# Performance work log

Hardware: AMD Instinct MI355X
Metric: run time of the kernel (lower is better)

The kernel has to match this reference:

```python
import jax, jax.numpy as jnp
import numpy as np

B, S, D, H = 2, 2048, 1024, 16
DK = D // H  # 64


def setup_inputs() -> dict:
    key = jax.random.key(0)
    ks = jax.random.split(key, 5)
    query_input = jax.random.normal(ks[0], (B, S, D), dtype=jnp.float32)
    # additive mask: 1.0 where attention is disallowed (causal upper triangle)
    mask = jnp.triu(jnp.ones((S, S), dtype=jnp.float32), k=1)[None, None, :, :]
    scale = 1.0 / np.sqrt(D)
    wq = jax.random.normal(ks[1], (D, D), dtype=jnp.float32) * scale
    wk = jax.random.normal(ks[2], (D, D), dtype=jnp.float32) * scale
    wv = jax.random.normal(ks[3], (D, D), dtype=jnp.float32) * scale
    wo = jax.random.normal(ks[4], (D, D), dtype=jnp.float32) * scale
    return {"query_input": query_input, "mask": mask, "wq": wq, "wk": wk, "wv": wv, "wo": wo}


def _split_heads(x):
    # [B, S, D] -> [B, H, S, DK]
    b, s, _ = x.shape
    return x.reshape(b, s, H, DK).transpose(0, 2, 1, 3)


def reference(query_input, mask, wq, wk, wv, wo):
    # self-attention: key_input = value_input = query_input
    q = _split_heads(query_input @ wq)  # [B, H, S, DK]
    k = _split_heads(query_input @ wk)
    v = _split_heads(query_input @ wv)
    scores = jnp.einsum('bhqd,bhkd->bhqk', q, k) / jnp.sqrt(jnp.float32(DK))
    scores = scores + mask * (-1e9)
    attn = jax.nn.softmax(scores, axis=-1)
    out = jnp.einsum('bhqk,bhkd->bhqd', attn, v)  # [B, H, S, DK]
    out = out.transpose(0, 2, 1, 3).reshape(query_input.shape[0], -1, D)
    return out @ wo
```

## Files before the change

kernel.cpp:

```cpp
#include <hip/hip_runtime.h>

typedef __attribute__((ext_vector_type(8))) short bf16x8;
typedef __attribute__((ext_vector_type(4))) float f32x4;
typedef __attribute__((ext_vector_type(4))) unsigned short u16x4;

#define S_LEN 2048
#define D_DIM 1024
#define NHEAD 16
#define DK 64
#define BH 32
#define MROWS 4096

__device__ __forceinline__ unsigned short f2bf(float f) {
    unsigned int u = __float_as_uint(f);
    u += 0x7fffu + ((u >> 16) & 1u);
    return (unsigned short)(u >> 16);
}

__device__ __forceinline__ void gload16(const void* g, void* l) {
    __builtin_amdgcn_global_load_lds(
        (const __attribute__((address_space(1))) void*)g,
        (__attribute__((address_space(3))) void*)l, 16, 0, 0);
}

__global__ __launch_bounds__(256) void cast_x_kernel(const float* __restrict__ X,
                                                     unsigned short* __restrict__ Xb) {
    int idx = blockIdx.x * 256 + threadIdx.x;
    float4 v = ((const float4*)X)[idx];
    u16x4 o;
    o.x = f2bf(v.x); o.y = f2bf(v.y); o.z = f2bf(v.z); o.w = f2bf(v.w);
    ((u16x4*)Xb)[idx] = o;
}

__global__ __launch_bounds__(256) void wtrans_kernel(const float* __restrict__ wq,
                                                     const float* __restrict__ wk,
                                                     const float* __restrict__ wv,
                                                     const float* __restrict__ wo,
                                                     unsigned short* __restrict__ Wt) {
    int z = blockIdx.z;
    const float* W = (z == 0) ? wq : (z == 1) ? wk : (z == 2) ? wv : wo;
    unsigned short* O = Wt + (size_t)z * D_DIM * D_DIM;
    __shared__ float t[32][33];
    int tx = threadIdx.x, ty = threadIdx.y;
    int bx = blockIdx.x * 32;
    int by = blockIdx.y * 32;
#pragma unroll
    for (int i = 0; i < 4; ++i)
        t[ty + i * 8][tx] = W[(size_t)(by + ty + i * 8) * D_DIM + bx + tx];
    __syncthreads();
#pragma unroll
    for (int i = 0; i < 4; ++i)
        O[(size_t)(bx + ty + i * 8) * D_DIM + by + tx] = f2bf(t[tx][ty + i * 8]);
}

__device__ __forceinline__ void gemm_mainloop(const unsigned short* __restrict__ A,
                                              const unsigned short* __restrict__ Bt,
                                              int K, int m0, int n0,
                                              unsigned short* As, unsigned short* Bs,
                                              f32x4 acc[4][4]) {
    const int tid = threadIdx.x;
    const int lane = tid & 63, wid = tid >> 6;
    const int wr = wid >> 1, wc = wid & 1;
    const int fr = lane & 15, fk = (lane >> 4) * 8;
    for (int k0 = 0; k0 < K; k0 += 32) {
        __syncthreads();
#pragma unroll
        for (int c = 0; c < 2; ++c) {
            int idx = c * 256 + tid;
            int row = idx >> 2;
            int col = (idx & 3) * 8;
            int base = (c * 256 + wid * 64) * 8;
            gload16(&A[(size_t)(m0 + row) * K + k0 + col], &As[base]);
            gload16(&Bt[(size_t)(n0 + row) * K + k0 + col], &Bs[base]);
        }
        __syncthreads();
        bf16x8 af[4], bfr[4];
#pragma unroll
        for (int i = 0; i < 4; ++i)
            af[i] = *(const bf16x8*)&As[(wr * 64 + i * 16 + fr) * 32 + fk];
#pragma unroll
        for (int j = 0; j < 4; ++j)
            bfr[j] = *(const bf16x8*)&Bs[(wc * 64 + j * 16 + fr) * 32 + fk];
#pragma unroll
        for (int i = 0; i < 4; ++i)
#pragma unroll
            for (int j = 0; j < 4; ++j)
                acc[i][j] = __builtin_amdgcn_mfma_f32_16x16x32_bf16(af[i], bfr[j], acc[i][j], 0, 0, 0);
    }
}

#define QSCALE 0.18033688011112042f
__global__ __launch_bounds__(256) void gemm_qkv_kernel(const unsigned short* __restrict__ Xb,
                                                       const unsigned short* __restrict__ Wt,
                                                       unsigned short* __restrict__ QKV) {
    __shared__ __align__(16) unsigned short As[128 * 32];
    __shared__ __align__(16) unsigned short Bs[128 * 32];
    const unsigned short* Bt = Wt + (size_t)blockIdx.z * D_DIM * D_DIM;
    unsigned short* Out = QKV + (size_t)blockIdx.z * MROWS * D_DIM;
    int m0 = blockIdx.y * 128, n0 = blockIdx.x * 128;
    f32x4 acc[4][4] = {};
    gemm_mainloop(Xb, Bt, D_DIM, m0, n0, As, Bs, acc);
    const float qs = (blockIdx.z == 0) ? QSCALE : 1.0f;
    const int lane = threadIdx.x & 63, wid = threadIdx.x >> 6;
    const int wr = wid >> 1, wc = wid & 1;
#pragma unroll
    for (int i = 0; i < 4; ++i)
#pragma unroll
        for (int j = 0; j < 4; ++j)
#pragma unroll
            for (int r = 0; r < 4; ++r) {
                int gm = m0 + wr * 64 + i * 16 + (lane >> 4) * 4 + r;
                int gn = n0 + wc * 64 + j * 16 + (lane & 15);
                int b = gm >> 11, s = gm & 2047, h = gn >> 6, dk = gn & 63;
                Out[((size_t)((b * NHEAD + h) * S_LEN + s)) * DK + dk] = f2bf(acc[i][j][r] * qs);
            }
}

__global__ __launch_bounds__(256) void vtrans_kernel(const unsigned short* __restrict__ V,
                                                     unsigned short* __restrict__ Vt) {
    __shared__ unsigned short tile[64][65];
    int bh = blockIdx.y;
    int s0 = blockIdx.x * 64;
    int t = threadIdx.x;
#pragma unroll
    for (int i = 0; i < 16; ++i) {
        int idx = i * 256 + t;
        int row = idx >> 6, col = idx & 63;
        tile[row][col] = V[((size_t)bh * S_LEN + s0 + row) * DK + col];
    }
    __syncthreads();
#pragma unroll
    for (int i = 0; i < 16; ++i) {
        int idx = i * 256 + t;
        int dr = idx >> 6, sc = idx & 63;
        Vt[((size_t)bh * DK + dr) * S_LEN + s0 + sc] = tile[sc][dr];
    }
}

__global__ __launch_bounds__(256) void attn_kernel(const unsigned short* __restrict__ QKV,
                                                   const unsigned short* __restrict__ Vt,
                                                   unsigned short* __restrict__ AO) {
    const int bh = blockIdx.y;
    const int tid = threadIdx.x, lane = tid & 63, wid = tid >> 6;
    const int fr = lane & 15, fkg = lane >> 4, fk = fkg * 8;
    const unsigned short* Q = QKV;
    const unsigned short* Kd = QKV + (size_t)MROWS * D_DIM;

    __shared__ __align__(16) unsigned short Ks[2][64][64];
    __shared__ __align__(16) unsigned short Vs[2][64][64];
    __shared__ __align__(16) unsigned short Ps[4][16][64];

    const int b = bh >> 4, h = bh & 15;
    const int rsw  = fr & 7;
    const int off0 = (fkg ^ rsw) * 8;
    const int off1 = ((4 + fkg) ^ rsw) * 8;

    for (int half = 0; half < 2; ++half) {
        const int qi = half ? (31 - (int)blockIdx.x) : (int)blockIdx.x;
        const int q0 = qi * 64;
        const int qr = q0 + wid * 16;

        bf16x8 qf0 = *(const bf16x8*)&Q[((size_t)bh * S_LEN + qr + fr) * DK + fk];
        bf16x8 qf1 = *(const bf16x8*)&Q[((size_t)bh * S_LEN + qr + fr) * DK + 32 + fk];

        f32x4 o[4] = {};
        float m = -1e30f, l = 0.f;
        const int ntiles = qi + 1;
        int buf = 0;

#pragma unroll
        for (int c = 0; c < 2; ++c) {
            int chunk = wid * 128 + c * 64 + lane;
            int row = chunk >> 3;
            int scol = ((chunk & 7) ^ (row & 7)) * 8;
            int base = (wid * 128 + c * 64) * 8;
            gload16(&Kd[((size_t)bh * S_LEN + row) * DK + scol], &Ks[0][0][0] + base);
            gload16(&Vt[((size_t)bh * DK + row) * S_LEN + scol], &Vs[0][0][0] + base);
        }
        __syncthreads();

        for (int t = 0; t < ntiles; ++t) {
            if (t + 1 < ntiles) {
                const int ktn = (t + 1) * 64;
#pragma unroll
                for (int c = 0; c < 2; ++c) {
                    int chunk = wid * 128 + c * 64 + lane;
                    int row = chunk >> 3;
                    int scol = ((chunk & 7) ^ (row & 7)) * 8;
                    int base = (wid * 128 + c * 64) * 8;
                    gload16(&Kd[((size_t)bh * S_LEN + ktn + row) * DK + scol], &Ks[buf ^ 1][0][0] + base);
                    gload16(&Vt[((size_t)bh * DK + row) * S_LEN + ktn + scol], &Vs[buf ^ 1][0][0] + base);
                }
            }

            f32x4 s4[4];
#pragma unroll
            for (int nj = 0; nj < 4; ++nj) {
                const unsigned short* krow = &Ks[buf][nj * 16 + fr][0];
                bf16x8 kf0 = *(const bf16x8*)&krow[off0];
                bf16x8 kf1 = *(const bf16x8*)&krow[off1];
                f32x4 z = {};
                z = __builtin_amdgcn_mfma_f32_16x16x32_bf16(kf0, qf0, z, 0, 0, 0);
                z = __builtin_amdgcn_mfma_f32_16x16x32_bf16(kf1, qf1, z, 0, 0, 0);
                s4[nj] = z;
            }

            if (t == ntiles - 1) {
                const int qoff = wid * 16 + fr;
#pragma unroll
                for (int nj = 0; nj < 4; ++nj)
#pragma unroll
                    for (int r = 0; r < 4; ++r)
                        s4[nj][r] = (nj * 16 + fkg * 4 + r > qoff) ? -1e30f : s4[nj][r];
            }

            float m0_ = fmaxf(fmaxf(s4[0][0], s4[0][1]), fmaxf(s4[0][2], s4[0][3]));
            float m1_ = fmaxf(fmaxf(s4[1][0], s4[1][1]), fmaxf(s4[1][2], s4[1][3]));
            float m2_ = fmaxf(fmaxf(s4[2][0], s4[2][1]), fmaxf(s4[2][2], s4[2][3]));
            float m3_ = fmaxf(fmaxf(s4[3][0], s4[3][1]), fmaxf(s4[3][2], s4[3][3]));
            float mt = fmaxf(fmaxf(m0_, m1_), fmaxf(m2_, m3_));
            mt = fmaxf(mt, __shfl_xor(mt, 16, 64));
            mt = fmaxf(mt, __shfl_xor(mt, 32, 64));
            float mn = fmaxf(m, mt);
            float corr = exp2f(m - mn);
            m = mn;
            float ps = 0.f;
            u16x4 pw[4];
#pragma unroll
            for (int nj = 0; nj < 4; ++nj) {
                float p0 = exp2f(s4[nj][0] - mn);
                float p1 = exp2f(s4[nj][1] - mn);
                float p2 = exp2f(s4[nj][2] - mn);
                float p3 = exp2f(s4[nj][3] - mn);
                ps += (p0 + p1) + (p2 + p3);
                pw[nj].x = f2bf(p0); pw[nj].y = f2bf(p1);
                pw[nj].z = f2bf(p2); pw[nj].w = f2bf(p3);
            }
            ps += __shfl_xor(ps, 16, 64);
            ps += __shfl_xor(ps, 32, 64);
            l = l * corr + ps;
#pragma unroll
            for (int j = 0; j < 4; ++j) o[j] *= corr;

#pragma unroll
            for (int nj = 0; nj < 4; ++nj) {
                int chunk = nj * 2 + (fkg >> 1);
                int el = (fkg & 1) * 4;
                *(u16x4*)&Ps[wid][fr][((chunk ^ rsw) << 3) + el] = pw[nj];
            }
            bf16x8 pf0 = *(const bf16x8*)&Ps[wid][fr][off0];
            bf16x8 pf1 = *(const bf16x8*)&Ps[wid][fr][off1];
#pragma unroll
            for (int j = 0; j < 4; ++j) {
                const unsigned short* vrow = &Vs[buf][j * 16 + fr][0];
                bf16x8 vf0 = *(const bf16x8*)&vrow[off0];
                bf16x8 vf1 = *(const bf16x8*)&vrow[off1];
                o[j] = __builtin_amdgcn_mfma_f32_16x16x32_bf16(vf0, pf0, o[j], 0, 0, 0);
                o[j] = __builtin_amdgcn_mfma_f32_16x16x32_bf16(vf1, pf1, o[j], 0, 0, 0);
            }

            __syncthreads();
            buf ^= 1;
        }

        float inv = 1.0f / l;
        size_t rowoff = ((size_t)(b * S_LEN) + qr + fr) * D_DIM + h * DK;
#pragma unroll
        for (int j = 0; j < 4; ++j) {
            u16x4 w;
            w.x = f2bf(o[j][0] * inv); w.y = f2bf(o[j][1] * inv);
            w.z = f2bf(o[j][2] * inv); w.w = f2bf(o[j][3] * inv);
            *(u16x4*)&AO[rowoff + j * 16 + fkg * 4] = w;
        }
    }
}

__global__ __launch_bounds__(256) void gemm_out_kernel(const unsigned short* __restrict__ AO,
                                                       const unsigned short* __restrict__ Wot,
                                                       float* __restrict__ out) {
    __shared__ __align__(16) unsigned short As[128 * 32];
    __shared__ __align__(16) unsigned short Bs[128 * 32];
    int m0 = blockIdx.y * 128, n0 = blockIdx.x * 128;
    f32x4 acc[4][4] = {};
    gemm_mainloop(AO, Wot, D_DIM, m0, n0, As, Bs, acc);
    const int lane = threadIdx.x & 63, wid = threadIdx.x >> 6;
    const int wr = wid >> 1, wc = wid & 1;
#pragma unroll
    for (int i = 0; i < 4; ++i)
#pragma unroll
        for (int j = 0; j < 4; ++j)
#pragma unroll
            for (int r = 0; r < 4; ++r) {
                int gm = m0 + wr * 64 + i * 16 + (lane >> 4) * 4 + r;
                int gn = n0 + wc * 64 + j * 16 + (lane & 15);
                out[(size_t)gm * D_DIM + gn] = acc[i][j][r];
            }
}

extern "C" void kernel_launch(void* const* d_in, const int* in_sizes, int n_in,
                              void* d_out, int out_size, void* d_ws, size_t ws_size,
                              hipStream_t stream) {
    (void)in_sizes; (void)n_in; (void)out_size; (void)ws_size;
    const float* X  = (const float*)d_in[0];
    const float* wq = (const float*)d_in[2];
    const float* wk = (const float*)d_in[3];
    const float* wv = (const float*)d_in[4];
    const float* wo = (const float*)d_in[5];

    char* ws = (char*)d_ws;
    unsigned short* Xb  = (unsigned short*)(ws);
    unsigned short* Wt  = (unsigned short*)(ws + ((size_t)8  << 20));
    unsigned short* QKV = (unsigned short*)(ws + ((size_t)16 << 20));
    unsigned short* Vt  = (unsigned short*)(ws + ((size_t)40 << 20));
    unsigned short* AO  = (unsigned short*)(ws + ((size_t)48 << 20));
    float* out = (float*)d_out;

    cast_x_kernel<<<4096, 256, 0, stream>>>(X, Xb);
    wtrans_kernel<<<dim3(32, 32, 4), dim3(32, 8), 0, stream>>>(wq, wk, wv, wo, Wt);
    gemm_qkv_kernel<<<dim3(8, 32, 3), 256, 0, stream>>>(Xb, Wt, QKV);
    vtrans_kernel<<<dim3(32, 32), 256, 0, stream>>>(QKV + (size_t)2 * MROWS * D_DIM, Vt);
    attn_kernel<<<dim3(16, 32), 256, 0, stream>>>(QKV, Vt, AO);
    gemm_out_kernel<<<dim3(8, 32), 256, 0, stream>>>(AO, Wt + (size_t)3 * D_DIM * D_DIM, out);
}
```

Baseline: 137.5 us.

## Split attention into one block per query tile, add lazy rescale and packed bf16 convert

The attention kernel now launches one block per (head, query tile) and orders tiles longest-first, instead of pairing a short and a long tile inside one block. This doubles the block count for better occupancy and load balance across CUs. Online-softmax rescaling is skipped unless the running max grows by more than a threshold, which saves exp and multiply work. Probabilities are converted with the packed v_cvt_pk_bf16_f32 instruction. The lazy rescale lets unnormalised values grow by up to 2^8 before correction, which slightly changes the numerics.

```diff
diff --git a/kernel.cpp b/kernel.cpp
--- a/kernel.cpp
+++ b/kernel.cpp
@@ -15,6 +15,12 @@
     unsigned int u = __float_as_uint(f);
     u += 0x7fffu + ((u >> 16) & 1u);
     return (unsigned short)(u >> 16);
+}
+
+__device__ __forceinline__ unsigned int pk_bf16(float a, float b) {
+    unsigned int r;
+    asm("v_cvt_pk_bf16_f32 %0, %1, %2" : "=v"(r) : "v"(a), "v"(b));
+    return r;
 }
 
 __device__ __forceinline__ void gload16(const void* g, void* l) {
@@ -140,7 +146,8 @@
 __global__ __launch_bounds__(256) void attn_kernel(const unsigned short* __restrict__ QKV,
                                                    const unsigned short* __restrict__ Vt,
                                                    unsigned short* __restrict__ AO) {
-    const int bh = blockIdx.y;
+    const int bh = blockIdx.x;
+    const int qi = 31 - (int)blockIdx.y;
     const int tid = threadIdx.x, lane = tid & 63, wid = tid >> 6;
     const int fr = lane & 15, fkg = lane >> 4, fk = fkg * 8;
     const unsigned short* Q = QKV;
@@ -155,123 +162,122 @@
     const int off0 = (fkg ^ rsw) * 8;
     const int off1 = ((4 + fkg) ^ rsw) * 8;
 
-    for (int half = 0; half < 2; ++half) {
-        const int qi = half ? (31 - (int)blockIdx.x) : (int)blockIdx.x;
-        const int q0 = qi * 64;
-        const int qr = q0 + wid * 16;
-
-        bf16x8 qf0 = *(const bf16x8*)&Q[((size_t)bh * S_LEN + qr + fr) * DK + fk];
-        bf16x8 qf1 = *(const bf16x8*)&Q[((size_t)bh * S_LEN + qr + fr) * DK + 32 + fk];
-
-        f32x4 o[4] = {};
-        float m = -1e30f, l = 0.f;
-        const int ntiles = qi + 1;
-        int buf = 0;
-
-#pragma unroll
-        for (int c = 0; c < 2; ++c) {
-            int chunk = wid * 128 + c * 64 + lane;
-            int row = chunk >> 3;
-            int scol = ((chunk & 7) ^ (row & 7)) * 8;
-            int base = (wid * 128 + c * 64) * 8;
-            gload16(&Kd[((size_t)bh * S_LEN + row) * DK + scol], &Ks[0][0][0] + base);
-            gload16(&Vt[((size_t)bh * DK + row) * S_LEN + scol], &Vs[0][0][0] + base);
-        }
-        __syncthreads();
-
-        for (int t = 0; t < ntiles; ++t) {
-            if (t + 1 < ntiles) {
-                const int ktn = (t + 1) * 64;
-#pragma unroll
-                for (int c = 0; c < 2; ++c) {
-                    int chunk = wid * 128 + c * 64 + lane;
-                    int row = chunk >> 3;
-                    int scol = ((chunk & 7) ^ (row & 7)) * 8;
-                    int base = (wid * 128 + c * 64) * 8;
-                    gload16(&Kd[((size_t)bh * S_LEN + ktn + row) * DK + scol], &Ks[buf ^ 1][0][0] + base);
-                    gload16(&Vt[((size_t)bh * DK + row) * S_LEN + ktn + scol], &Vs[buf ^ 1][0][0] + base);
-                }
+    const int q0 = qi * 64;
+    const int qr = q0 + wid * 16;
+
+    bf16x8 qf0 = *(const bf16x8*)&Q[((size_t)bh * S_LEN + qr + fr) * DK + fk];
+    bf16x8 qf1 = *(const bf16x8*)&Q[((size_t)bh * S_LEN + qr + fr) * DK + 32 + fk];
+
+    f32x4 o[4] = {};
+    float m = -1e30f, l = 0.f;
+    const int ntiles = qi + 1;
+    int buf = 0;
+
+#pragma unroll
+    for (int c = 0; c < 2; ++c) {
+        int chunk = wid * 128 + c * 64 + lane;
+        int row = chunk >> 3;
+        int scol = ((chunk & 7) ^ (row & 7)) * 8;
+        int base = (wid * 128 + c * 64) * 8;
+        gload16(&Kd[((size_t)bh * S_LEN + row) * DK + scol], &Ks[0][0][0] + base);
+        gload16(&Vt[((size_t)bh * DK + row) * S_LEN + scol], &Vs[0][0][0] + base);
+    }
+    __syncthreads();
+
+    for (int t = 0; t < ntiles; ++t) {
+        if (t + 1 < ntiles) {
+            const int ktn = (t + 1) * 64;
+#pragma unroll
+            for (int c = 0; c < 2; ++c) {
+                int chunk = wid * 128 + c * 64 + lane;
+                int row = chunk >> 3;
+                int scol = ((chunk & 7) ^ (row & 7)) * 8;
+                int base = (wid * 128 + c * 64) * 8;
+                gload16(&Kd[((size_t)bh * S_LEN + ktn + row) * DK + scol], &Ks[buf ^ 1][0][0] + base);
+                gload16(&Vt[((size_t)bh * DK + row) * S_LEN + ktn + scol], &Vs[buf ^ 1][0][0] + base);
             }
-
-            f32x4 s4[4];
-#pragma unroll
-            for (int nj = 0; nj < 4; ++nj) {
-                const unsigned short* krow = &Ks[buf][nj * 16 + fr][0];
-                bf16x8 kf0 = *(const bf16x8*)&krow[off0];
-                bf16x8 kf1 = *(const bf16x8*)&krow[off1];
-                f32x4 z = {};
-                z = __builtin_amdgcn_mfma_f32_16x16x32_bf16(kf0, qf0, z, 0, 0, 0);
-                z = __builtin_amdgcn_mfma_f32_16x16x32_bf16(kf1, qf1, z, 0, 0, 0);
-                s4[nj] = z;
-            }
-
-            if (t == ntiles - 1) {
-                const int qoff = wid * 16 + fr;
-#pragma unroll
-                for (int nj = 0; nj < 4; ++nj)
-#pragma unroll
-                    for (int r = 0; r < 4; ++r)
-                        s4[nj][r] = (nj * 16 + fkg * 4 + r > qoff) ? -1e30f : s4[nj][r];
-            }
-
-            float m0_ = fmaxf(fmaxf(s4[0][0], s4[0][1]), fmaxf(s4[0][2], s4[0][3]));
-            float m1_ = fmaxf(fmaxf(s4[1][0], s4[1][1]), fmaxf(s4[1][2], s4[1][3]));
-            float m2_ = fmaxf(fmaxf(s4[2][0], s4[2][1]), fmaxf(s4[2][2], s4[2][3]));
-            float m3_ = fmaxf(fmaxf(s4[3][0], s4[3][1]), fmaxf(s4[3][2], s4[3][3]));
-            float mt = fmaxf(fmaxf(m0_, m1_), fmaxf(m2_, m3_));
-            mt = fmaxf(mt, __shfl_xor(mt, 16, 64));
-            mt = fmaxf(mt, __shfl_xor(mt, 32, 64));
+        }
+
+        f32x4 s4[4];
+#pragma unroll
+        for (int nj = 0; nj < 4; ++nj) {
+            const unsigned short* krow = &Ks[buf][nj * 16 + fr][0];
+            bf16x8 kf0 = *(const bf16x8*)&krow[off0];
+            bf16x8 kf1 = *(const bf16x8*)&krow[off1];
+            f32x4 z = {};
+            z = __builtin_amdgcn_mfma_f32_16x16x32_bf16(kf0, qf0, z, 0, 0, 0);
+            z = __builtin_amdgcn_mfma_f32_16x16x32_bf16(kf1, qf1, z, 0, 0, 0);
+            s4[nj] = z;
+        }
+
+        if (t == ntiles - 1) {
+            const int qoff = wid * 16 + fr;
+#pragma unroll
+            for (int nj = 0; nj < 4; ++nj)
+#pragma unroll
+                for (int r = 0; r < 4; ++r)
+                    s4[nj][r] = (nj * 16 + fkg * 4 + r > qoff) ? -1e30f : s4[nj][r];
+        }
+
+        float m0_ = fmaxf(fmaxf(s4[0][0], s4[0][1]), fmaxf(s4[0][2], s4[0][3]));
+        float m1_ = fmaxf(fmaxf(s4[1][0], s4[1][1]), fmaxf(s4[1][2], s4[1][3]));
+        float m2_ = fmaxf(fmaxf(s4[2][0], s4[2][1]), fmaxf(s4[2][2], s4[2][3]));
+        float m3_ = fmaxf(fmaxf(s4[3][0], s4[3][1]), fmaxf(s4[3][2], s4[3][3]));
+        float mt = fmaxf(fmaxf(m0_, m1_), fmaxf(m2_, m3_));
+        mt = fmaxf(mt, __shfl_xor(mt, 16, 64));
+        mt = fmaxf(mt, __shfl_xor(mt, 32, 64));
+        if (!__all(mt <= m + 8.0f)) {
             float mn = fmaxf(m, mt);
             float corr = exp2f(m - mn);
             m = mn;
-            float ps = 0.f;
-            u16x4 pw[4];
-#pragma unroll
-            for (int nj = 0; nj < 4; ++nj) {
-                float p0 = exp2f(s4[nj][0] - mn);
-                float p1 = exp2f(s4[nj][1] - mn);
-                float p2 = exp2f(s4[nj][2] - mn);
-                float p3 = exp2f(s4[nj][3] - mn);
-                ps += (p0 + p1) + (p2 + p3);
-                pw[nj].x = f2bf(p0); pw[nj].y = f2bf(p1);
-                pw[nj].z = f2bf(p2); pw[nj].w = f2bf(p3);
-            }
-            ps += __shfl_xor(ps, 16, 64);
-            ps += __shfl_xor(ps, 32, 64);
-            l = l * corr + ps;
-#pragma unroll
-            for (int j = 0; j < 4; ++j) o[j] *= corr;
-
-#pragma unroll
-            for (int nj = 0; nj < 4; ++nj) {
-                int chunk = nj * 2 + (fkg >> 1);
-                int el = (fkg & 1) * 4;
-                *(u16x4*)&Ps[wid][fr][((chunk ^ rsw) << 3) + el] = pw[nj];
-            }
-            bf16x8 pf0 = *(const bf16x8*)&Ps[wid][fr][off0];
-            bf16x8 pf1 = *(const bf16x8*)&Ps[wid][fr][off1];
-#pragma unroll
-            for (int j = 0; j < 4; ++j) {
-                const unsigned short* vrow = &Vs[buf][j * 16 + fr][0];
-                bf16x8 vf0 = *(const bf16x8*)&vrow[off0];
-                bf16x8 vf1 = *(const bf16x8*)&vrow[off1];
-                o[j] = __builtin_amdgcn_mfma_f32_16x16x32_bf16(vf0, pf0, o[j], 0, 0, 0);
-                o[j] = __builtin_amdgcn_mfma_f32_16x16x32_bf16(vf1, pf1, o[j], 0, 0, 0);
-            }
-
-            __syncthreads();
-            buf ^= 1;
-        }
-
-        float inv = 1.0f / l;
-        size_t rowoff = ((size_t)(b * S_LEN) + qr + fr) * D_DIM + h * DK;
+            l *= corr;
+            o[0] *= corr; o[1] *= corr; o[2] *= corr; o[3] *= corr;
+        }
+        float ps = 0.f;
+        unsigned int pw[4][2];
+#pragma unroll
+        for (int nj = 0; nj < 4; ++nj) {
+            float p0 = exp2f(s4[nj][0] - m);
+            float p1 = exp2f(s4[nj][1] - m);
+            float p2 = exp2f(s4[nj][2] - m);
+            float p3 = exp2f(s4[nj][3] - m);
+            ps += (p0 + p1) + (p2 + p3);
+            pw[nj][0] = pk_bf16(p0, p1);
+            pw[nj][1] = pk_bf16(p2, p3);
+        }
+        ps += __shfl_xor(ps, 16, 64);
+        ps += __shfl_xor(ps, 32, 64);
+        l += ps;
+
+#pragma unroll
+        for (int nj = 0; nj < 4; ++nj) {
+            int chunk = nj * 2 + (fkg >> 1);
+            int el = (fkg & 1) * 4;
+            *(uint2*)&Ps[wid][fr][((chunk ^ rsw) << 3) + el] = make_uint2(pw[nj][0], pw[nj][1]);
+        }
+        bf16x8 pf0 = *(const bf16x8*)&Ps[wid][fr][off0];
+        bf16x8 pf1 = *(const bf16x8*)&Ps[wid][fr][off1];
 #pragma unroll
         for (int j = 0; j < 4; ++j) {
-            u16x4 w;
-            w.x = f2bf(o[j][0] * inv); w.y = f2bf(o[j][1] * inv);
-            w.z = f2bf(o[j][2] * inv); w.w = f2bf(o[j][3] * inv);
-            *(u16x4*)&AO[rowoff + j * 16 + fkg * 4] = w;
-        }
+            const unsigned short* vrow = &Vs[buf][j * 16 + fr][0];
+            bf16x8 vf0 = *(const bf16x8*)&vrow[off0];
+            bf16x8 vf1 = *(const bf16x8*)&vrow[off1];
+            o[j] = __builtin_amdgcn_mfma_f32_16x16x32_bf16(vf0, pf0, o[j], 0, 0, 0);
+            o[j] = __builtin_amdgcn_mfma_f32_16x16x32_bf16(vf1, pf1, o[j], 0, 0, 0);
+        }
+
+        __syncthreads();
+        buf ^= 1;
+    }
+
+    float inv = 1.0f / l;
+    size_t rowoff = ((size_t)(b * S_LEN) + qr + fr) * D_DIM + h * DK;
+#pragma unroll
+    for (int j = 0; j < 4; ++j) {
+        u16x4 w;
+        w.x = f2bf(o[j][0] * inv); w.y = f2bf(o[j][1] * inv);
+        w.z = f2bf(o[j][2] * inv); w.w = f2bf(o[j][3] * inv);
+        *(u16x4*)&AO[rowoff + j * 16 + fkg * 4] = w;
     }
 }
 
@@ -319,6 +325,6 @@
     wtrans_kernel<<<dim3(32, 32, 4), dim3(32, 8), 0, stream>>>(wq, wk, wv, wo, Wt);
     gemm_qkv_kernel<<<dim3(8, 32, 3), 256, 0, stream>>>(Xb, Wt, QKV);
     vtrans_kernel<<<dim3(32, 32), 256, 0, stream>>>(QKV + (size_t)2 * MROWS * D_DIM, Vt);
-    attn_kernel<<<dim3(16, 32), 256, 0, stream>>>(QKV, Vt, AO);
+    attn_kernel<<<dim3(32, 32), 256, 0, stream>>>(QKV, Vt, AO);
     gemm_out_kernel<<<dim3(8, 32), 256, 0, stream>>>(AO, Wt + (size_t)3 * D_DIM * D_DIM, out);
 }
```

Result: faster. 123.0 us (-10.6%).
